# Optimization experiments

Measured on AMD Instinct MI355X. Metric: run time of the kernel, lower is better.

## Reference

```python
import jax, jax.numpy as jnp
import numpy as np

B, S, C, H = 2, 2048, 1024, 16
D = C // H  # head_size = 64


def setup_inputs() -> dict:
    key = jax.random.key(0)
    ks = jax.random.split(key, 8)
    scale = 1.0 / np.sqrt(C)
    return {
        "src": jax.random.normal(ks[0], (B, S, C), dtype=jnp.float32),
        "Wq": jax.random.normal(ks[1], (C, C), dtype=jnp.float32) * scale,
        "bq": jnp.zeros((C,), dtype=jnp.float32),
        "Wk": jax.random.normal(ks[2], (C, C), dtype=jnp.float32) * scale,
        "bk": jnp.zeros((C,), dtype=jnp.float32),
        "Wv": jax.random.normal(ks[3], (C, C), dtype=jnp.float32) * scale,
        "bv": jnp.zeros((C,), dtype=jnp.float32),
        "rel_k_table": jax.random.normal(ks[4], (2 * S - 1, D), dtype=jnp.float32),
    }


def reference(src, Wq, bq, Wk, bk, Wv, bv, rel_k_table):
    # Linear projections (torch Linear: x @ W.T + b)
    q = src @ Wq.T + bq  # (B,S,C)
    k = src @ Wk.T + bk
    v = src @ Wv.T + bv
    # Faithful to torch .view: raw reshape (B,S,C) -> (B,H,S,D), NOT a transpose split
    q = q.reshape(B, H, S, D)
    k = k.reshape(B, H, S, D)
    v = v.reshape(B, H, S, D)
    # content score: q @ k^T
    content = jnp.einsum("bhsd,bhtd->bhst", q, k)  # (B,H,S,S)
    # relative-position embeddings: (S,S,D)
    pos = jnp.arange(S)
    shifted = pos[None, :] - pos[:, None] + (S - 1)  # (S,S) in [0, 2S-2]
    rel_k = rel_k_table[shifted]  # (S,S,D)
    # q.view(S, B*H, D) @ rel_k.permute(0,2,1): batched over first (query-pos) axis
    q_r = q.reshape(S, B * H, D)
    pos_score = jnp.einsum("sbd,std->sbt", q_r, rel_k)  # (S,BH,S)
    pos_score = jnp.transpose(pos_score, (1, 0, 2)).reshape(B, H, S, S)
    scores = (content + pos_score) / jnp.sqrt(jnp.float32(D))
    attn = jax.nn.softmax(scores, axis=-1)
    out = jnp.einsum("bhst,bhtd->bhsd", attn, v)  # (B,H,S,D)
    out = jnp.transpose(out, (0, 2, 1, 3)).reshape(B, S, C)
    return out
```

## Files before the change

### kernel.cpp

```cpp
#include <hip/hip_runtime.h>
#include <hip/hip_bf16.h>

#define BATCH 2
#define SEQ   2048
#define CH    1024
#define NH    16
#define HD    64
#define BHN   (BATCH*NH)
#define SD    (SEQ*HD)

typedef short v8s __attribute__((ext_vector_type(8)));
typedef short v4s __attribute__((ext_vector_type(4)));
typedef float v4f __attribute__((ext_vector_type(4)));

__device__ __forceinline__ short f2bf(float f) {
    unsigned u = __float_as_uint(f);
    u += 0x7fff + ((u >> 16) & 1);
    return (short)(u >> 16);
}

__device__ __forceinline__ unsigned pk2bf(float a, float b) {
    __hip_bfloat162 h = __float22bfloat162_rn(make_float2(a, b));
    unsigned u;
    __builtin_memcpy(&u, &h, 4);
    return u;
}

__device__ __forceinline__ float ex2(float x) {
    float r; asm("v_exp_f32 %0, %1" : "=v"(r) : "v"(x)); return r;
}

#if __has_builtin(__builtin_amdgcn_perm)
#define PERMB(a, b, s) __builtin_amdgcn_perm((a), (b), (s))
#else
__device__ __forceinline__ unsigned PERMB(unsigned a, unsigned b, unsigned s) {
    unsigned r = 0;
#pragma unroll
    for (int i = 0; i < 4; i++) {
        unsigned sb = (s >> (8 * i)) & 0xff, byte;
        if (sb >= 12) byte = (sb == 12) ? 0u : 0xffu;
        else if (sb < 4) byte = (b >> (8 * sb)) & 0xff;
        else byte = (a >> (8 * (sb - 4))) & 0xff;
        r |= byte << (8 * i);
    }
    return r;
}
#endif

__device__ __forceinline__ void gl_lds16(const short* g, short* l) {
    __builtin_amdgcn_global_load_lds(
        (const __attribute__((address_space(1))) void*)g,
        (__attribute__((address_space(3))) void*)l, 16, 0, 0);
}

__global__ __launch_bounds__(256) void cast_all_kernel(
    const float* __restrict__ src, const float* __restrict__ wq,
    const float* __restrict__ wk, const float* __restrict__ wv,
    const float* __restrict__ rel,
    short* __restrict__ xb, short* __restrict__ wqb,
    short* __restrict__ wkb, short* __restrict__ wvb,
    short* __restrict__ relb)
{
    const int z = blockIdx.z;
    const float* s; short* d; int n4;
    switch (z) {
        case 0: s = src; d = xb;   n4 = 1048576; break;
        case 1: s = wq;  d = wqb;  n4 = 262144;  break;
        case 2: s = wk;  d = wkb;  n4 = 262144;  break;
        case 3: s = wv;  d = wvb;  n4 = 262144;  break;
        default: s = rel; d = relb; n4 = 65520;  break;
    }
    for (int i = blockIdx.x * 256 + threadIdx.x; i < n4; i += gridDim.x * 256) {
        float4 v = ((const float4*)s)[i];
        v4s o; o.x = f2bf(v.x); o.y = f2bf(v.y); o.z = f2bf(v.z); o.w = f2bf(v.w);
        ((v4s*)d)[i] = o;
    }
}

__global__ __launch_bounds__(256, 3) void proj_mfma_kernel(
    const short* __restrict__ Xb,
    const short* __restrict__ Wqb, const short* __restrict__ Wkb,
    const short* __restrict__ Wvb,
    const float* __restrict__ bq, const float* __restrict__ bk,
    const float* __restrict__ bv,
    short* __restrict__ qo, short* __restrict__ ko, short* __restrict__ vo)
{
    const int z = blockIdx.z;
    const short* W    = (z == 0) ? Wqb : (z == 1) ? Wkb : Wvb;
    const float* bias = (z == 0) ? bq  : (z == 1) ? bk  : bv;
    short*       out  = (z == 0) ? qo  : (z == 1) ? ko  : vo;
    const float  osc  = (z == 0) ? 0.125f * 1.44269504088896f : 1.0f;

    const int m0 = blockIdx.x * 128;
    const int n0 = blockIdx.y * 128;
    const int tid  = threadIdx.x;
    const int w    = tid >> 6;
    const int lane = tid & 63;
    const int l15  = lane & 15;
    const int quad = lane >> 4;
    const int wm = w & 1, wn = w >> 1;

    __shared__ short Al[128 * 32];
    __shared__ short Bl[128 * 32];

    v4f acc[4][4];
#pragma unroll
    for (int i = 0; i < 4; i++)
#pragma unroll
        for (int j = 0; j < 4; j++) acc[i][j] = (v4f)(0.f);

    const int lr = lane >> 2;
    const int lc = (lane & 3) * 8;

    for (int k0 = 0; k0 < 1024; k0 += 32) {
        __syncthreads();
#pragma unroll
        for (int l = 0; l < 2; l++) {
            const int slab = w * 32 + l * 16;
            gl_lds16(Xb + (size_t)(m0 + slab + lr) * 1024 + k0 + lc,
                     &Al[slab * 32]);
            gl_lds16(W + (size_t)(n0 + slab + lr) * 1024 + k0 + lc,
                     &Bl[slab * 32]);
        }
        __syncthreads();
        v8s af[4], bf[4];
#pragma unroll
        for (int mt = 0; mt < 4; mt++)
            af[mt] = *(const v8s*)&Al[(wm * 64 + mt * 16 + l15) * 32 + quad * 8];
#pragma unroll
        for (int nt = 0; nt < 4; nt++)
            bf[nt] = *(const v8s*)&Bl[(wn * 64 + nt * 16 + l15) * 32 + quad * 8];
#pragma unroll
        for (int mt = 0; mt < 4; mt++)
#pragma unroll
            for (int nt = 0; nt < 4; nt++)
                acc[mt][nt] = __builtin_amdgcn_mfma_f32_16x16x32_bf16(
                    af[mt], bf[nt], acc[mt][nt], 0, 0, 0);
    }

    float bv4[4];
#pragma unroll
    for (int nt = 0; nt < 4; nt++)
        bv4[nt] = bias[n0 + wn * 64 + nt * 16 + l15];
#pragma unroll
    for (int mt = 0; mt < 4; mt++)
#pragma unroll
        for (int rg = 0; rg < 4; rg++) {
            const int row = m0 + wm * 64 + mt * 16 + quad * 4 + rg;
#pragma unroll
            for (int nt = 0; nt < 4; nt++)
                out[(size_t)row * 1024 + n0 + wn * 64 + nt * 16 + l15] =
                    f2bf((acc[mt][nt][rg] + bv4[nt]) * osc);
        }
}

__global__ __launch_bounds__(256) void vtrans_kernel(
    const short* __restrict__ v, short* __restrict__ vt)
{
    const int bh = blockIdx.y;
    const int t0 = blockIdx.x * 64;
    const int r = threadIdx.x >> 3;
    const int c = (threadIdx.x & 7) * 8;

    __shared__ short T[64][72];
    *(v8s*)&T[r][c] =
        *(const v8s*)(v + (size_t)bh * SD + (size_t)(t0 + r) * HD + c);
    *(v8s*)&T[r + 32][c] =
        *(const v8s*)(v + (size_t)bh * SD + (size_t)(t0 + r + 32) * HD + c);
    __syncthreads();
    v8s o0, o1;
#pragma unroll
    for (int e = 0; e < 8; e++) {
        const int t = 2 * (threadIdx.x & 7) + (e >> 2) + 16 * (e & 3);
        o0[e] = T[t][r];
        o1[e] = T[t][r + 32];
    }
    *(v8s*)(vt + (size_t)bh * SD + (size_t)r * SEQ + t0 + c) = o0;
    *(v8s*)(vt + (size_t)bh * SD + (size_t)(r + 32) * SEQ + t0 + c) = o1;
}

__global__ __launch_bounds__(512, 4) void attn_mfma_kernel(
    const short* __restrict__ qb, const short* __restrict__ kb,
    const short* __restrict__ vtb, const short* __restrict__ relb,
    float* __restrict__ out)
{
    const int tid  = threadIdx.x;
    const int w    = tid >> 6;
    const int lane = tid & 63;
    const int l15  = lane & 15;
    const int quad = lane >> 4;
    const int bh = blockIdx.x, b = bh >> 4, h = bh & 15;
    const int s0 = blockIdx.y * 128;
    const int i0 = w * 16;

    __shared__ short Kl[2][64][64];
    __shared__ short Vl[2][64][64];
    __shared__ short Rl[256][64];
    __shared__ short Pb[8][16][64];

    v8s qc_f[2], qr_f[2];
#pragma unroll
    for (int kh = 0; kh < 2; kh++) {
        const int row = s0 + i0 + l15;
        qc_f[kh] = *(const v8s*)(qb + (size_t)bh * SD +
                                 (size_t)row * HD + kh * 32 + quad * 8);
        qr_f[kh] = *(const v8s*)(qb + (size_t)row * (BHN * HD) +
                                 bh * HD + kh * 32 + quad * 8);
    }

    int      slv4[4];
    unsigned selA[4], selB[4], pwoff[4];
#pragma unroll
    for (int rg = 0; rg < 4; rg++) {
        const int ii = quad * 4 + rg;
        const int e  = l15 + 15 - ii;
        const bool lo = (e < 16);
        slv4[rg] = (quad * 16 + (e & 15)) << 2;
        selA[rg] = lo ? 0x05040c0cu : 0x07060c0cu;
        selB[rg] = lo ? 0x07060c0cu : 0x01000c0cu;
        pwoff[rg] = (unsigned)(w * 2048 + ii * 128 +
                    ((((l15 >> 1) ^ (ii & 7)) << 4) + ((l15 & 1) << 3)));
    }

    const int swz = (quad ^ (l15 & 7)) << 4;
    int kaddr[2][4], paddr[2];
#pragma unroll
    for (int kh = 0; kh < 2; kh++) {
        const int x = kh << 6;
#pragma unroll
        for (int nt = 0; nt < 4; nt++)
            kaddr[kh][nt] = (((nt * 16 + l15) << 7) + swz) ^ x;
        paddr[kh] = ((l15 << 7) + swz) ^ x;
    }

    const int Bq = 1920 - s0;
    int raddr[5];
#pragma unroll
    for (int jt = 0; jt < 5; jt++) {
        const int lg = 2032 - s0 - i0 + jt * 16 + l15;
        raddr[jt] = ((lg & 255) << 7) + ((quad ^ (lg & 7)) << 4);
    }

    const int strow = tid >> 3;
    const int stc   = ((tid & 7) ^ (strow & 7)) * 8;
    const short* ksrc = kb  + (size_t)bh * SD + (size_t)strow * HD  + stc;
    const short* vsrc = vtb + (size_t)bh * SD + (size_t)strow * SEQ + stc;

#pragma unroll
    for (int g = 0; g < 3; g++) {
        const int lr2 = Bq + g * 64 + strow;
        const int cr = lr2 < 4094 ? lr2 : 4094;
        gl_lds16(relb + (size_t)cr * HD + stc,
                 &Rl[(Bq + g * 64 + w * 8) & 255][0]);
    }
    gl_lds16(ksrc, &Kl[0][w * 8][0]);
    gl_lds16(vsrc, &Vl[0][w * 8][0]);

    const short* kp = ksrc + 4096;
    const short* vp = vsrc + 64;
    const char*  relbp = (const char*)relb + stc * 2;
    unsigned roff = (unsigned)(Bq + 192 + strow) * 128;
    const unsigned ROMAX = 4094u * 128;
    unsigned rlds = (unsigned)((Bq + 192 + w * 8) & 255) << 7;

    v4f o_acc[4];
#pragma unroll
    for (int nt = 0; nt < 4; nt++) o_acc[nt] = (v4f)(0.f);
    float lpart[4] = {0.f, 0.f, 0.f, 0.f};

    int cur = 0;
    for (int t0 = 0; t0 < SEQ; t0 += 64, cur ^= 1) {
        __syncthreads();

        {
            short* kd = &Kl[0][w * 8][0];
            short* vd = &Vl[0][w * 8][0];
            const int nb = (cur ^ 1) << 12;
            gl_lds16(kp, kd + nb);
            gl_lds16(vp, vd + nb);
            unsigned rc = roff < ROMAX ? roff : ROMAX;
            gl_lds16((const short*)(relbp + rc), (short*)((char*)Rl + rlds));
        }
        kp += 4096; vp += 64; roff += 8192;
        rlds = (rlds + 8192) & 32767;

        v4f cacc[4], racc[5];
#pragma unroll
        for (int nt = 0; nt < 4; nt++) cacc[nt] = (v4f)(0.f);
#pragma unroll
        for (int jt = 0; jt < 5; jt++) racc[jt] = (v4f)(0.f);

        const char* kbase = (const char*)Kl + cur * 8192;
        const char* vbase = (const char*)Vl + cur * 8192;
        const char* rbase = (const char*)Rl;

#pragma unroll
        for (int kh = 0; kh < 2; kh++) {
            v8s kf[4], rfj[5];
#pragma unroll
            for (int nt = 0; nt < 4; nt++)
                kf[nt] = *(const v8s*)(kbase + kaddr[kh][nt]);
#pragma unroll
            for (int jt = 0; jt < 5; jt++)
                rfj[jt] = *(const v8s*)(rbase + (raddr[jt] ^ (kh << 6)));
            __builtin_amdgcn_s_setprio(1);
#pragma unroll
            for (int nt = 0; nt < 4; nt++)
                cacc[nt] = __builtin_amdgcn_mfma_f32_16x16x32_bf16(
                    qc_f[kh], kf[nt], cacc[nt], 0, 0, 0);
#pragma unroll
            for (int jt = 0; jt < 5; jt++)
                racc[jt] = __builtin_amdgcn_mfma_f32_16x16x32_bf16(
                    qr_f[kh], rfj[jt], racc[jt], 0, 0, 0);
            __builtin_amdgcn_s_setprio(0);
        }
#pragma unroll
        for (int jt = 0; jt < 5; jt++) raddr[jt] = (raddr[jt] + 8192) & 32767;

        unsigned g01[4], g23[4], g4v[4];
#pragma unroll
        for (int rg = 0; rg < 4; rg++) {
            unsigned p01 = pk2bf(racc[0][rg], racc[1][rg]);
            unsigned p23 = pk2bf(racc[2][rg], racc[3][rg]);
            unsigned p4  = pk2bf(racc[4][rg], racc[4][rg]);
            g01[rg] = (unsigned)__builtin_amdgcn_ds_bpermute(slv4[rg], (int)p01);
            g23[rg] = (unsigned)__builtin_amdgcn_ds_bpermute(slv4[rg], (int)p23);
            g4v[rg] = (unsigned)__builtin_amdgcn_ds_bpermute(slv4[rg], (int)p4);
        }
#pragma unroll
        for (int rg = 0; rg < 4; rg++) {
            const unsigned a01 = g01[rg], a23 = g23[rg], a4 = g4v[rg];
            unsigned pb0 = PERMB(a01, a01, selA[rg]);
            unsigned pb1 = PERMB(a01, a23, selB[rg]);
            unsigned pb2 = PERMB(a23, a23, selA[rg]);
            unsigned pb3 = PERMB(a23, a4,  selB[rg]);
            float p0 = ex2(cacc[0][rg] + __uint_as_float(pb0));
            float p1 = ex2(cacc[1][rg] + __uint_as_float(pb1));
            float p2 = ex2(cacc[2][rg] + __uint_as_float(pb2));
            float p3 = ex2(cacc[3][rg] + __uint_as_float(pb3));
            lpart[rg] += (p0 + p1) + (p2 + p3);
            *(uint2*)((char*)Pb + pwoff[rg]) =
                make_uint2(pk2bf(p0, p1), pk2bf(p2, p3));
        }

        const char* pbase = (const char*)Pb + w * 2048;
#pragma unroll
        for (int kh = 0; kh < 2; kh++) {
            v8s pa = *(const v8s*)(pbase + paddr[kh]);
            __builtin_amdgcn_s_setprio(1);
#pragma unroll
            for (int nt = 0; nt < 4; nt++) {
                v8s vf = *(const v8s*)(vbase + kaddr[kh][nt]);
                o_acc[nt] = __builtin_amdgcn_mfma_f32_16x16x32_bf16(
                    pa, vf, o_acc[nt], 0, 0, 0);
            }
            __builtin_amdgcn_s_setprio(0);
        }
    }

#pragma unroll
    for (int rg = 0; rg < 4; rg++) {
        float rs = lpart[rg];
#pragma unroll
        for (int off = 1; off < 16; off <<= 1)
            rs += __shfl_xor(rs, off);
        const float inv = 1.f / rs;
        const int row = s0 + i0 + quad * 4 + rg;
        const size_t base = ((size_t)b * SEQ + row) * CH + h * HD;
#pragma unroll
        for (int nt = 0; nt < 4; nt++)
            out[base + nt * 16 + l15] = o_acc[nt][rg] * inv;
    }
}

extern "C" void kernel_launch(void* const* d_in, const int* in_sizes, int n_in,
                              void* d_out, int out_size, void* d_ws, size_t ws_size,
                              hipStream_t stream)
{
    const float* src  = (const float*)d_in[0];
    const float* Wq   = (const float*)d_in[1];
    const float* bq   = (const float*)d_in[2];
    const float* Wk   = (const float*)d_in[3];
    const float* bk   = (const float*)d_in[4];
    const float* Wv   = (const float*)d_in[5];
    const float* bv   = (const float*)d_in[6];
    const float* relk = (const float*)d_in[7];
    float* out = (float*)d_out;

    const size_t nQKV = (size_t)BATCH * SEQ * CH;
    const size_t nW   = (size_t)CH * CH;
    short* qb   = (short*)d_ws;
    short* kb   = qb + nQKV;
    short* vb   = kb + nQKV;
    short* vtb  = vb + nQKV;
    short* xb   = vtb + nQKV;
    short* wqb  = xb + nQKV;
    short* wkb  = wqb + nW;
    short* wvb  = wkb + nW;
    short* relb = wvb + nW;

    cast_all_kernel<<<dim3(512, 1, 5), 256, 0, stream>>>(
        src, Wq, Wk, Wv, relk, xb, wqb, wkb, wvb, relb);

    dim3 gProj(4096 / 128, 1024 / 128, 3);
    proj_mfma_kernel<<<gProj, 256, 0, stream>>>(
        xb, wqb, wkb, wvb, bq, bk, bv, qb, kb, vb);

    dim3 gVt(SEQ / 64, BHN);
    vtrans_kernel<<<gVt, 256, 0, stream>>>(vb, vtb);

    dim3 gAttn(BHN, SEQ / 128);
    attn_mfma_kernel<<<gAttn, 512, 0, stream>>>(qb, kb, vtb, relb, out);
}
```

Baseline: 238.2 us.

## Give each attention wave two 16-row query tiles and halve block threads

The attention kernel now runs 4 waves of 256 threads per block instead of 8 waves, and each wave handles 32 query rows as two 16-row M tiles. K, V and relative-position fragments loaded from LDS are reused across both tiles, and the two tiles share an overlapping window of 6 rel-k fragments instead of 5 each. This cuts LDS reads per MFMA and per-wave overhead, but raises register pressure, which drops occupancy, and each thread now issues twice as many global-to-LDS loads.

```diff
diff --git a/kernel.cpp b/kernel.cpp
--- a/kernel.cpp
+++ b/kernel.cpp
@@ -179,7 +179,7 @@
     *(v8s*)(vt + (size_t)bh * SD + (size_t)(r + 32) * SEQ + t0 + c) = o1;
 }
 
-__global__ __launch_bounds__(512, 4) void attn_mfma_kernel(
+__global__ __launch_bounds__(256, 2) void attn_mfma_kernel(
     const short* __restrict__ qb, const short* __restrict__ kb,
     const short* __restrict__ vtb, const short* __restrict__ relb,
     float* __restrict__ out)
@@ -191,21 +191,23 @@
     const int quad = lane >> 4;
     const int bh = blockIdx.x, b = bh >> 4, h = bh & 15;
     const int s0 = blockIdx.y * 128;
-    const int i0 = w * 16;
+    const int i0 = w * 32;
 
     __shared__ short Kl[2][64][64];
     __shared__ short Vl[2][64][64];
     __shared__ short Rl[256][64];
-    __shared__ short Pb[8][16][64];
-
-    v8s qc_f[2], qr_f[2];
+    __shared__ short Pb[4][2][16][64];
+
+    v8s qc_f[2][2], qr_f[2][2];
+#pragma unroll
+    for (int mt = 0; mt < 2; mt++)
 #pragma unroll
     for (int kh = 0; kh < 2; kh++) {
-        const int row = s0 + i0 + l15;
-        qc_f[kh] = *(const v8s*)(qb + (size_t)bh * SD +
-                                 (size_t)row * HD + kh * 32 + quad * 8);
-        qr_f[kh] = *(const v8s*)(qb + (size_t)row * (BHN * HD) +
-                                 bh * HD + kh * 32 + quad * 8);
+        const int row = s0 + i0 + mt * 16 + l15;
+        qc_f[mt][kh] = *(const v8s*)(qb + (size_t)bh * SD +
+                                     (size_t)row * HD + kh * 32 + quad * 8);
+        qr_f[mt][kh] = *(const v8s*)(qb + (size_t)row * (BHN * HD) +
+                                     bh * HD + kh * 32 + quad * 8);
     }
 
     int      slv4[4];
@@ -218,27 +220,27 @@
         slv4[rg] = (quad * 16 + (e & 15)) << 2;
         selA[rg] = lo ? 0x05040c0cu : 0x07060c0cu;
         selB[rg] = lo ? 0x07060c0cu : 0x01000c0cu;
-        pwoff[rg] = (unsigned)(w * 2048 + ii * 128 +
+        pwoff[rg] = (unsigned)(w * 4096 + ii * 128 +
                     ((((l15 >> 1) ^ (ii & 7)) << 4) + ((l15 & 1) << 3)));
     }
 
     const int swz = (quad ^ (l15 & 7)) << 4;
-    int kaddr[2][4], paddr[2];
+    int kaddr[2][4];
 #pragma unroll
     for (int kh = 0; kh < 2; kh++) {
         const int x = kh << 6;
 #pragma unroll
         for (int nt = 0; nt < 4; nt++)
             kaddr[kh][nt] = (((nt * 16 + l15) << 7) + swz) ^ x;
-        paddr[kh] = ((l15 << 7) + swz) ^ x;
-    }
+    }
+    const int paddr0 = (l15 << 7) + swz;
 
     const int Bq = 1920 - s0;
-    int raddr[5];
-#pragma unroll
-    for (int jt = 0; jt < 5; jt++) {
-        const int lg = 2032 - s0 - i0 + jt * 16 + l15;
-        raddr[jt] = ((lg & 255) << 7) + ((quad ^ (lg & 7)) << 4);
+    int raddr[6];
+#pragma unroll
+    for (int st = 0; st < 6; st++) {
+        const int lg = 2032 - s0 - i0 - 16 + st * 16 + l15;
+        raddr[st] = ((lg & 255) << 7) + ((quad ^ (lg & 7)) << 4);
     }
 
     const int strow = tid >> 3;
@@ -248,13 +250,17 @@
 
 #pragma unroll
     for (int g = 0; g < 3; g++) {
-        const int lr2 = Bq + g * 64 + strow;
-        const int cr = lr2 < 4094 ? lr2 : 4094;
-        gl_lds16(relb + (size_t)cr * HD + stc,
-                 &Rl[(Bq + g * 64 + w * 8) & 255][0]);
-    }
-    gl_lds16(ksrc, &Kl[0][w * 8][0]);
-    gl_lds16(vsrc, &Vl[0][w * 8][0]);
+        const int r0 = Bq + g * 64 + strow;
+        const int ra = r0 < 4094 ? r0 : 4094;
+        const int rb2 = (r0 + 32) < 4094 ? (r0 + 32) : 4094;
+        const unsigned sl = (unsigned)((Bq + g * 64 + w * 8) & 255) << 7;
+        gl_lds16(relb + (size_t)ra * HD + stc, (short*)((char*)Rl + sl));
+        gl_lds16(relb + (size_t)rb2 * HD + stc, (short*)((char*)Rl + sl + 4096));
+    }
+    gl_lds16(ksrc,              &Kl[0][w * 8][0]);
+    gl_lds16(ksrc + 32 * HD,    &Kl[0][32 + w * 8][0]);
+    gl_lds16(vsrc,              &Vl[0][w * 8][0]);
+    gl_lds16(vsrc + 32 * SEQ,   &Vl[0][32 + w * 8][0]);
 
     const short* kp = ksrc + 4096;
     const short* vp = vsrc + 64;
@@ -263,32 +269,41 @@
     const unsigned ROMAX = 4094u * 128;
     unsigned rlds = (unsigned)((Bq + 192 + w * 8) & 255) << 7;
 
-    v4f o_acc[4];
-#pragma unroll
-    for (int nt = 0; nt < 4; nt++) o_acc[nt] = (v4f)(0.f);
-    float lpart[4] = {0.f, 0.f, 0.f, 0.f};
+    v4f o_acc[2][4];
+#pragma unroll
+    for (int mt = 0; mt < 2; mt++)
+#pragma unroll
+        for (int nt = 0; nt < 4; nt++) o_acc[mt][nt] = (v4f)(0.f);
+    float lpart[2][4] = {{0.f,0.f,0.f,0.f},{0.f,0.f,0.f,0.f}};
 
     int cur = 0;
     for (int t0 = 0; t0 < SEQ; t0 += 64, cur ^= 1) {
         __syncthreads();
 
         {
-            short* kd = &Kl[0][w * 8][0];
-            short* vd = &Vl[0][w * 8][0];
             const int nb = (cur ^ 1) << 12;
-            gl_lds16(kp, kd + nb);
-            gl_lds16(vp, vd + nb);
-            unsigned rc = roff < ROMAX ? roff : ROMAX;
-            gl_lds16((const short*)(relbp + rc), (short*)((char*)Rl + rlds));
+            short* kd = &Kl[0][w * 8][0] + nb;
+            short* vd = &Vl[0][w * 8][0] + nb;
+            gl_lds16(kp,            kd);
+            gl_lds16(kp + 32 * HD,  kd + 32 * 64);
+            gl_lds16(vp,            vd);
+            gl_lds16(vp + 32 * SEQ, vd + 32 * 64);
+            unsigned rc0 = roff < ROMAX ? roff : ROMAX;
+            unsigned rc1 = (roff + 4096) < ROMAX ? (roff + 4096) : ROMAX;
+            gl_lds16((const short*)(relbp + rc0), (short*)((char*)Rl + rlds));
+            gl_lds16((const short*)(relbp + rc1), (short*)((char*)Rl + rlds + 4096));
         }
         kp += 4096; vp += 64; roff += 8192;
         rlds = (rlds + 8192) & 32767;
 
-        v4f cacc[4], racc[5];
-#pragma unroll
-        for (int nt = 0; nt < 4; nt++) cacc[nt] = (v4f)(0.f);
-#pragma unroll
-        for (int jt = 0; jt < 5; jt++) racc[jt] = (v4f)(0.f);
+        v4f cacc[2][4], racc[2][5];
+#pragma unroll
+        for (int mt = 0; mt < 2; mt++) {
+#pragma unroll
+            for (int nt = 0; nt < 4; nt++) cacc[mt][nt] = (v4f)(0.f);
+#pragma unroll
+            for (int jt = 0; jt < 5; jt++) racc[mt][jt] = (v4f)(0.f);
+        }
 
         const char* kbase = (const char*)Kl + cur * 8192;
         const char* vbase = (const char*)Vl + cur * 8192;
@@ -296,80 +311,99 @@
 
 #pragma unroll
         for (int kh = 0; kh < 2; kh++) {
-            v8s kf[4], rfj[5];
+            v8s kf[4], rfj[6];
 #pragma unroll
             for (int nt = 0; nt < 4; nt++)
                 kf[nt] = *(const v8s*)(kbase + kaddr[kh][nt]);
 #pragma unroll
+            for (int st = 0; st < 6; st++)
+                rfj[st] = *(const v8s*)(rbase + (raddr[st] ^ (kh << 6)));
+            __builtin_amdgcn_s_setprio(1);
+#pragma unroll
+            for (int mt = 0; mt < 2; mt++)
+#pragma unroll
+                for (int nt = 0; nt < 4; nt++)
+                    cacc[mt][nt] = __builtin_amdgcn_mfma_f32_16x16x32_bf16(
+                        qc_f[mt][kh], kf[nt], cacc[mt][nt], 0, 0, 0);
+#pragma unroll
             for (int jt = 0; jt < 5; jt++)
-                rfj[jt] = *(const v8s*)(rbase + (raddr[jt] ^ (kh << 6)));
-            __builtin_amdgcn_s_setprio(1);
-#pragma unroll
-            for (int nt = 0; nt < 4; nt++)
-                cacc[nt] = __builtin_amdgcn_mfma_f32_16x16x32_bf16(
-                    qc_f[kh], kf[nt], cacc[nt], 0, 0, 0);
+                racc[0][jt] = __builtin_amdgcn_mfma_f32_16x16x32_bf16(
+                    qr_f[0][kh], rfj[jt + 1], racc[0][jt], 0, 0, 0);
 #pragma unroll
             for (int jt = 0; jt < 5; jt++)
-                racc[jt] = __builtin_amdgcn_mfma_f32_16x16x32_bf16(
-                    qr_f[kh], rfj[jt], racc[jt], 0, 0, 0);
+                racc[1][jt] = __builtin_amdgcn_mfma_f32_16x16x32_bf16(
+                    qr_f[1][kh], rfj[jt], racc[1][jt], 0, 0, 0);
             __builtin_amdgcn_s_setprio(0);
         }
 #pragma unroll
-        for (int jt = 0; jt < 5; jt++) raddr[jt] = (raddr[jt] + 8192) & 32767;
-
-        unsigned g01[4], g23[4], g4v[4];
+        for (int st = 0; st < 6; st++) raddr[st] = (raddr[st] + 8192) & 32767;
+
+        unsigned g01[2][4], g23[2][4], g4v[2][4];
+#pragma unroll
+        for (int mt = 0; mt < 2; mt++)
 #pragma unroll
         for (int rg = 0; rg < 4; rg++) {
-            unsigned p01 = pk2bf(racc[0][rg], racc[1][rg]);
-            unsigned p23 = pk2bf(racc[2][rg], racc[3][rg]);
-            unsigned p4  = pk2bf(racc[4][rg], racc[4][rg]);
-            g01[rg] = (unsigned)__builtin_amdgcn_ds_bpermute(slv4[rg], (int)p01);
-            g23[rg] = (unsigned)__builtin_amdgcn_ds_bpermute(slv4[rg], (int)p23);
-            g4v[rg] = (unsigned)__builtin_amdgcn_ds_bpermute(slv4[rg], (int)p4);
-        }
+            unsigned p01 = pk2bf(racc[mt][0][rg], racc[mt][1][rg]);
+            unsigned p23 = pk2bf(racc[mt][2][rg], racc[mt][3][rg]);
+            unsigned p4  = pk2bf(racc[mt][4][rg], racc[mt][4][rg]);
+            g01[mt][rg] = (unsigned)__builtin_amdgcn_ds_bpermute(slv4[rg], (int)p01);
+            g23[mt][rg] = (unsigned)__builtin_amdgcn_ds_bpermute(slv4[rg], (int)p23);
+            g4v[mt][rg] = (unsigned)__builtin_amdgcn_ds_bpermute(slv4[rg], (int)p4);
+        }
+#pragma unroll
+        for (int mt = 0; mt < 2; mt++)
 #pragma unroll
         for (int rg = 0; rg < 4; rg++) {
-            const unsigned a01 = g01[rg], a23 = g23[rg], a4 = g4v[rg];
+            const unsigned a01 = g01[mt][rg], a23 = g23[mt][rg], a4 = g4v[mt][rg];
             unsigned pb0 = PERMB(a01, a01, selA[rg]);
             unsigned pb1 = PERMB(a01, a23, selB[rg]);
             unsigned pb2 = PERMB(a23, a23, selA[rg]);
             unsigned pb3 = PERMB(a23, a4,  selB[rg]);
-            float p0 = ex2(cacc[0][rg] + __uint_as_float(pb0));
-            float p1 = ex2(cacc[1][rg] + __uint_as_float(pb1));
-            float p2 = ex2(cacc[2][rg] + __uint_as_float(pb2));
-            float p3 = ex2(cacc[3][rg] + __uint_as_float(pb3));
-            lpart[rg] += (p0 + p1) + (p2 + p3);
-            *(uint2*)((char*)Pb + pwoff[rg]) =
+            float p0 = ex2(cacc[mt][0][rg] + __uint_as_float(pb0));
+            float p1 = ex2(cacc[mt][1][rg] + __uint_as_float(pb1));
+            float p2 = ex2(cacc[mt][2][rg] + __uint_as_float(pb2));
+            float p3 = ex2(cacc[mt][3][rg] + __uint_as_float(pb3));
+            lpart[mt][rg] += (p0 + p1) + (p2 + p3);
+            *(uint2*)((char*)Pb + pwoff[rg] + mt * 2048) =
                 make_uint2(pk2bf(p0, p1), pk2bf(p2, p3));
         }
 
-        const char* pbase = (const char*)Pb + w * 2048;
+        const char* pbW = (const char*)Pb + w * 4096;
 #pragma unroll
         for (int kh = 0; kh < 2; kh++) {
-            v8s pa = *(const v8s*)(pbase + paddr[kh]);
+            v8s vf[4];
+#pragma unroll
+            for (int nt = 0; nt < 4; nt++)
+                vf[nt] = *(const v8s*)(vbase + kaddr[kh][nt]);
+            v8s pa0 = *(const v8s*)(pbW + (paddr0 ^ (kh << 6)));
+            v8s pa1 = *(const v8s*)(pbW + 2048 + (paddr0 ^ (kh << 6)));
             __builtin_amdgcn_s_setprio(1);
 #pragma unroll
-            for (int nt = 0; nt < 4; nt++) {
-                v8s vf = *(const v8s*)(vbase + kaddr[kh][nt]);
-                o_acc[nt] = __builtin_amdgcn_mfma_f32_16x16x32_bf16(
-                    pa, vf, o_acc[nt], 0, 0, 0);
-            }
+            for (int nt = 0; nt < 4; nt++)
+                o_acc[0][nt] = __builtin_amdgcn_mfma_f32_16x16x32_bf16(
+                    pa0, vf[nt], o_acc[0][nt], 0, 0, 0);
+#pragma unroll
+            for (int nt = 0; nt < 4; nt++)
+                o_acc[1][nt] = __builtin_amdgcn_mfma_f32_16x16x32_bf16(
+                    pa1, vf[nt], o_acc[1][nt], 0, 0, 0);
             __builtin_amdgcn_s_setprio(0);
         }
     }
 
 #pragma unroll
+    for (int mt = 0; mt < 2; mt++)
+#pragma unroll
     for (int rg = 0; rg < 4; rg++) {
-        float rs = lpart[rg];
+        float rs = lpart[mt][rg];
 #pragma unroll
         for (int off = 1; off < 16; off <<= 1)
             rs += __shfl_xor(rs, off);
         const float inv = 1.f / rs;
-        const int row = s0 + i0 + quad * 4 + rg;
+        const int row = s0 + i0 + mt * 16 + quad * 4 + rg;
         const size_t base = ((size_t)b * SEQ + row) * CH + h * HD;
 #pragma unroll
         for (int nt = 0; nt < 4; nt++)
-            out[base + nt * 16 + l15] = o_acc[nt][rg] * inv;
+            out[base + nt * 16 + l15] = o_acc[mt][nt][rg] * inv;
     }
 }
 
@@ -410,5 +444,5 @@
     vtrans_kernel<<<gVt, 256, 0, stream>>>(vb, vtb);
 
     dim3 gAttn(BHN, SEQ / 128);
-    attn_mfma_kernel<<<gAttn, 512, 0, stream>>>(qb, kb, vtb, relb, out);
-}
+    attn_mfma_kernel<<<gAttn, 256, 0, stream>>>(qb, kb, vtb, relb, out);
+}
```

Measured after the change: 209.5 us. -12.1%, faster.
